# Kernel optimization log

Measured on AMD Instinct MI355X. Metric: run time of the kernel, lower is better.

## Reference

```python
import jax, jax.numpy as jnp
import numpy as np

N, NN, NI, ND, NH = 20000, 32, 128, 128, 8
RADIUS = 1.0
EPS = 1e-5


def _mlp(x, W1, b1, W2, b2):
    return jax.nn.elu(x @ W1 + b1) @ W2 + b2


def setup_inputs() -> dict:
    key = jax.random.key(0)
    ks = jax.random.split(key, 32)
    s = 0.05
    inp = {
        "features": jax.random.normal(ks[0], (N, NI), jnp.float32),
        "x": jax.random.normal(ks[1], (N, 3), jnp.float32),
        "nuv": jax.random.normal(ks[2], (N, 3, 3), jnp.float32),
        "topk": jax.random.randint(ks[3], (N, NN), 0, N, jnp.int64),
        # query_f: Ni -> Nd -> Nh*Nd
        "qW1": jax.random.normal(ks[4], (NI, ND), jnp.float32) * s,
        "qb1": jnp.zeros((ND,), jnp.float32),
        "qW2": jax.random.normal(ks[5], (ND, NH * ND), jnp.float32) * s,
        "qb2": jnp.zeros((NH * ND,), jnp.float32),
        # geo_encoder: 12 -> Nd -> Nd
        "gW1": jax.random.normal(ks[6], (12, ND), jnp.float32) * s,
        "gb1": jnp.zeros((ND,), jnp.float32),
        "gW2": jax.random.normal(ks[7], (ND, ND), jnp.float32) * s,
        "gb2": jnp.zeros((ND,), jnp.float32),
        # key_f / value_f: Nd -> Nd -> Nd
        "kW1": jax.random.normal(ks[8], (ND, ND), jnp.float32) * s,
        "kb1": jnp.zeros((ND,), jnp.float32),
        "kW2": jax.random.normal(ks[9], (ND, ND), jnp.float32) * s,
        "kb2": jnp.zeros((ND,), jnp.float32),
        "vW1": jax.random.normal(ks[10], (ND, ND), jnp.float32) * s,
        "vb1": jnp.zeros((ND,), jnp.float32),
        "vW2": jax.random.normal(ks[11], (ND, ND), jnp.float32) * s,
        "vb2": jnp.zeros((ND,), jnp.float32),
        # decode_f: Nh*Nd -> Nd -> Nd
        "dW1": jax.random.normal(ks[12], (NH * ND, ND), jnp.float32) * s,
        "db1": jnp.zeros((ND,), jnp.float32),
        "dW2": jax.random.normal(ks[13], (ND, ND), jnp.float32) * s,
        "db2": jnp.zeros((ND,), jnp.float32),
        # LayerNorm
        "ln_g": jnp.ones((ND,), jnp.float32),
        "ln_b": jnp.zeros((ND,), jnp.float32),
    }
    return inp


def reference(features, x, nuv, topk, qW1, qb1, qW2, qb2, gW1, gb1, gW2, gb2,
              kW1, kb1, kW2, kb2, vW1, vb1, vW2, vb2, dW1, db1, dW2, db2,
              ln_g, ln_b):
    n, nn = topk.shape
    sdk = jnp.sqrt(jnp.float32(ND))

    Q = _mlp(features, qW1, qb1, qW2, qb2).reshape(n, NH, ND)  # (N,Nh,Nd)

    features_nn = features[topk]              # (N,nn,Nd)
    x_nn = x[topk]                            # (N,nn,3)
    orient_x = x_nn - x[:, None, :]           # (N,nn,3)
    nuv_nn = nuv[topk].reshape(n, nn * 3, 3)  # (N,nn*3,3)

    dis2 = jnp.sum(orient_x * orient_x, axis=2, keepdims=True)
    dis = jnp.exp(-dis2 / (2.0 * RADIUS * RADIUS))  # (N,nn,1)

    # rotate neighbor offsets / frames into local frame: nuv @ v^T, then transpose
    RL_x = jnp.einsum('nij,nkj->nki', nuv, orient_x)            # (N,nn,3)
    RL_nuv = jnp.einsum('nij,nkj->nki', nuv, nuv_nn)            # (N,nn*3,3)
    RL_nuv = RL_nuv.reshape(n, nn, 9)
    RL = jnp.concatenate([RL_x, RL_nuv], axis=-1)               # (N,nn,12)

    geo_fea = _mlp(RL, gW1, gb1, gW2, gb2)
    geo_fea = dis * geo_fea * features_nn                       # (N,nn,Nd)

    K = _mlp(geo_fea, kW1, kb1, kW2, kb2)                       # (N,nn,Nd)
    V = _mlp(geo_fea, vW1, vb1, vW2, vb2)                       # (N,nn,Nd)

    Mq = jnp.einsum('nhd,nkd->nhk', Q, K)                       # (N,Nh,nn)
    mask = (topk == 0)[:, None, :]                              # (N,1,nn)
    Mq = jnp.where(mask, -jnp.inf, Mq)
    Mq = jax.nn.softmax(Mq / sdk, axis=2)

    out = jnp.einsum('nhk,nkd->nhd', Mq, V).reshape(n, NH * ND)
    out = _mlp(out, dW1, db1, dW2, db2) + features

    mu = jnp.mean(out, axis=-1, keepdims=True)
    var = jnp.var(out, axis=-1, keepdims=True)
    return (out - mu) / jnp.sqrt(var + EPS) * ln_g + ln_b
```

## Files before the change

kernel.cpp:

```cpp
#include <hip/hip_runtime.h>
#include <math.h>
#include <stdint.h>

#define ND 128
#define NNB 32
#define NH 8

typedef __attribute__((ext_vector_type(8))) short bf16x8;
typedef __attribute__((ext_vector_type(4))) float f32x4;
typedef __attribute__((ext_vector_type(8))) unsigned short u16x8;
typedef unsigned short u16;
typedef unsigned int u32;
typedef unsigned long long u64;

#define OFF_QW1T 0ULL
#define OFF_QW2T 32768ULL
#define OFF_GW1T 294912ULL
#define OFF_GW2T 303104ULL
#define OFF_KW1T 335872ULL
#define OFF_KW2T 368640ULL
#define OFF_VW1T 401408ULL
#define OFF_VW2T 434176ULL
#define OFF_DW1T 466944ULL
#define OFF_DW2T 729088ULL
#define OFF_Q    761856ULL
#define OFF_ATT  (OFF_Q + 20096ULL * 2048ULL)

__device__ __forceinline__ u16 rneb(float f){
    u32 u = __builtin_bit_cast(u32, f);
    u32 r = u + 0x7fffu + ((u >> 16) & 1u);
    return (u16)(r >> 16);
}
__device__ __forceinline__ float elu_f(float v){ return v > 0.f ? v : (__expf(v) - 1.f); }
__device__ __forceinline__ u64 pack4(float a, float b, float c, float d){
    return (u64)rneb(a) | ((u64)rneb(b) << 16) | ((u64)rneb(c) << 32) | ((u64)rneb(d) << 48);
}

#define GLDS16(g, l) __builtin_amdgcn_global_load_lds( \
    (const __attribute__((address_space(1))) u32*)(g), \
    (__attribute__((address_space(3))) u32*)(u32)(u64)(l), 16, 0, 0)

__device__ __forceinline__ void stage_rows(char* lds, const char* g, size_t gstride){
    const int t = threadIdx.x;
    const int seg = (t & 15) * 16, rr = t >> 4;
    #pragma unroll
    for (int i = 0; i < 8; i++){
        int row = i * 16 + rr;
        GLDS16(g + (size_t)row * gstride + seg, lds + row * 256 + seg);
    }
}

__device__ __forceinline__ bf16x8 ldfrag(const u16* base, int row, int kb, int l){
    int r = row + (l & 15);
    int byte = (r << 8) + (((kb << 1) + ((l >> 4) << 4)) ^ ((r & 7) << 4));
    return *(const bf16x8*)((const char*)base + byte);
}
__device__ __forceinline__ bf16x8 ldfragG(const char* __restrict__ Wt, int n, int kstride, int kb, int l){
    return *(const bf16x8*)(Wt + (size_t)(n + (l & 15)) * (size_t)kstride
                               + (size_t)((kb << 1) + ((l >> 4) << 4)));
}
__device__ __forceinline__ bf16x8 ldfragRL(const u16* base, int row, int l){
    int r = row + (l & 15);
    int byte = (r << 6) + ((((l >> 4) << 4)) ^ ((r & 3) << 4));
    return *(const bf16x8*)((const char*)base + byte);
}

__device__ __forceinline__ void gemm_WA(const char* __restrict__ Wt, int kstride, int kbase,
                                        const u16* B, f32x4 acc[4][4]){
    const int t = threadIdx.x, l = t & 63;
    const int m0 = ((t >> 7) & 1) * 64;
    const int n0 = ((t >> 6) & 1) * 64;
    bf16x8 aw[4][4];
    #pragma unroll
    for (int kk = 0; kk < 4; kk++)
        #pragma unroll
        for (int i = 0; i < 4; i++)
            aw[kk][i] = ldfragG(Wt, m0 + i * 16, kstride, kbase + kk * 32, l);
    __builtin_amdgcn_s_setprio(1);
    #pragma unroll
    for (int kk = 0; kk < 4; kk++){
        bf16x8 b[4];
        #pragma unroll
        for (int i = 0; i < 4; i++) b[i] = ldfrag(B, n0 + i * 16, kk * 32, l);
        #pragma unroll
        for (int mt = 0; mt < 4; mt++)
            #pragma unroll
            for (int nt = 0; nt < 4; nt++)
                acc[mt][nt] = __builtin_amdgcn_mfma_f32_16x16x32_bf16(aw[kk][mt], b[nt], acc[mt][nt], 0, 0, 0);
    }
    __builtin_amdgcn_s_setprio(0);
}

__device__ __forceinline__ void gemm_AW(const u16* A, const char* __restrict__ Wt,
                                        f32x4 acc[4][4]){
    const int t = threadIdx.x, l = t & 63;
    const int m0 = ((t >> 7) & 1) * 64;
    const int n0 = ((t >> 6) & 1) * 64;
    bf16x8 bw[4][4];
    #pragma unroll
    for (int kk = 0; kk < 4; kk++)
        #pragma unroll
        for (int i = 0; i < 4; i++)
            bw[kk][i] = ldfragG(Wt, n0 + i * 16, 256, kk * 32, l);
    __builtin_amdgcn_s_setprio(1);
    #pragma unroll
    for (int kk = 0; kk < 4; kk++){
        bf16x8 a[4];
        #pragma unroll
        for (int i = 0; i < 4; i++) a[i] = ldfrag(A, m0 + i * 16, kk * 32, l);
        #pragma unroll
        for (int mt = 0; mt < 4; mt++)
            #pragma unroll
            for (int nt = 0; nt < 4; nt++)
                acc[mt][nt] = __builtin_amdgcn_mfma_f32_16x16x32_bf16(a[mt], bw[kk][nt], acc[mt][nt], 0, 0, 0);
    }
    __builtin_amdgcn_s_setprio(0);
}

struct PrepDesc {
    const float* src[10];
    u64 dstoff[10];
    int N[10], Ksrc[10], Kdst[10];
};

__global__ __launch_bounds__(256) void prep_weights(PrepDesc d, char* ws){
    int tid = blockIdx.x * 256 + threadIdx.x;
    #pragma unroll 1
    for (int m = 0; m < 10; m++){
        int cnt = (d.Kdst[m] * d.N[m]) >> 3;
        if (tid < cnt){
            int N = d.N[m];
            int nn = tid % N, k8 = tid / N;
            const float* s = d.src[m];
            u16x8 pk;
            #pragma unroll
            for (int i = 0; i < 8; i++){
                int k = k8 * 8 + i;
                pk[i] = (k < d.Ksrc[m]) ? rneb(s[(size_t)k * N + nn]) : (u16)0;
            }
            *(u16x8*)(ws + d.dstoff[m] + (u64)nn * (u64)(d.Kdst[m] * 2) + (u64)(k8 * 16)) = pk;
            return;
        }
        tid -= cnt;
    }
}

__global__ __launch_bounds__(256, 2) void qmlp_kernel(
    const float* __restrict__ F, const float* __restrict__ qb1, const float* __restrict__ qb2,
    const char* __restrict__ ws, u16* __restrict__ Qg, int n)
{
    __shared__ __align__(16) u16 sIn[16384];
    __shared__ __align__(16) u16 sH[16384];
    const int t = threadIdx.x;
    const int row0 = blockIdx.x * 128;
    const int l = t & 63;
    const int m0 = ((t >> 7) & 1) * 64;
    const int n0 = ((t >> 6) & 1) * 64;
    const int hi = l >> 4;

    for (int i = t; i < 4096; i += 256){
        int r = i >> 5, c = (i & 31) * 4;
        int gr = row0 + r;
        float4 v = make_float4(0.f, 0.f, 0.f, 0.f);
        if (gr < n) v = *(const float4*)&F[(size_t)gr * ND + c];
        *(u64*)((char*)sIn + (r << 8) + (((c << 1)) ^ ((r & 7) << 4))) = pack4(v.x, v.y, v.z, v.w);
    }
    __syncthreads();

    f32x4 acc[4][4];
    #pragma unroll
    for (int i = 0; i < 4; i++)
        #pragma unroll
        for (int j = 0; j < 4; j++) acc[i][j] = 0.f;
    gemm_WA(ws + OFF_QW1T, 256, 0, sIn, acc);
    #pragma unroll
    for (int mt = 0; mt < 4; mt++){
        int ch0 = m0 + mt * 16 + (hi << 2);
        float4 bq = *(const float4*)&qb1[ch0];
        #pragma unroll
        for (int nt = 0; nt < 4; nt++){
            int xrow = n0 + nt * 16 + (l & 15);
            u64 pk = pack4(elu_f(acc[mt][nt][0] + bq.x), elu_f(acc[mt][nt][1] + bq.y),
                           elu_f(acc[mt][nt][2] + bq.z), elu_f(acc[mt][nt][3] + bq.w));
            *(u64*)((char*)sH + (xrow << 8) + (((ch0 << 1)) ^ ((xrow & 7) << 4))) = pk;
        }
    }
    __syncthreads();

    for (int ct = 0; ct < 8; ct++){
        f32x4 a2[4][4];
        #pragma unroll
        for (int i = 0; i < 4; i++)
            #pragma unroll
            for (int j = 0; j < 4; j++) a2[i][j] = 0.f;
        gemm_WA(ws + OFF_QW2T + (u64)ct * 32768ULL, 256, 0, sH, a2);
        #pragma unroll
        for (int mt = 0; mt < 4; mt++){
            int ch0 = m0 + mt * 16 + (hi << 2);
            float4 bq = *(const float4*)&qb2[ct * 128 + ch0];
            #pragma unroll
            for (int nt = 0; nt < 4; nt++){
                int xrow = n0 + nt * 16 + (l & 15);
                *(u64*)((char*)sIn + (xrow << 8) + (ch0 << 1)) =
                    pack4(a2[mt][nt][0] + bq.x, a2[mt][nt][1] + bq.y,
                          a2[mt][nt][2] + bq.z, a2[mt][nt][3] + bq.w);
            }
        }
        __syncthreads();
        {
            int row = t >> 1, half = t & 1;
            int gr = row0 + row;
            if (gr < n){
                const char* src = (const char*)sIn + (row << 8) + half * 128;
                char* dst = (char*)Qg + (size_t)gr * 2048 + ct * 256 + half * 128;
                #pragma unroll
                for (int i = 0; i < 8; i++)
                    *(uint4*)(dst + i * 16) = *(const uint4*)(src + i * 16);
            }
        }
        __syncthreads();
    }
}

template<int ACT, bool INPLACE>
__device__ __forceinline__ void layerW(
    const u16* inB, u16* outB, const char* __restrict__ Wt,
    const float* __restrict__ bias, const float* __restrict__ F,
    const int* sidx, const float* sdis)
{
    const int t = threadIdx.x, l = t & 63;
    const int m0 = ((t >> 7) & 1) * 64;
    const int n0 = ((t >> 6) & 1) * 64;
    const int hi = l >> 4;
    f32x4 acc[4][4];
    #pragma unroll
    for (int i = 0; i < 4; i++)
        #pragma unroll
        for (int j = 0; j < 4; j++) acc[i][j] = 0.f;
    gemm_WA(Wt, 256, 0, inB, acc);
    if (INPLACE) __syncthreads();
    #pragma unroll
    for (int mt = 0; mt < 4; mt++){
        int ch0 = m0 + mt * 16 + (hi << 2);
        float4 bq = *(const float4*)&bias[ch0];
        #pragma unroll
        for (int nt = 0; nt < 4; nt++){
            int xrow = n0 + nt * 16 + (l & 15);
            float v[4];
            #pragma unroll
            for (int j = 0; j < 4; j++) v[j] = acc[mt][nt][j] + ((const float*)&bq)[j];
            if (ACT == 1){
                #pragma unroll
                for (int j = 0; j < 4; j++) v[j] = elu_f(v[j]);
            }
            if (ACT == 2){
                float dsc = sdis[xrow];
                float4 fq = *(const float4*)&F[(size_t)sidx[xrow] * ND + ch0];
                #pragma unroll
                for (int j = 0; j < 4; j++) v[j] *= dsc * ((const float*)&fq)[j];
            }
            *(u64*)((char*)outB + (xrow << 8) + (((ch0 << 1)) ^ ((xrow & 7) << 4))) =
                pack4(v[0], v[1], v[2], v[3]);
        }
    }
    __syncthreads();
}

__global__ __launch_bounds__(256, 2) void attn_kernel(
    const float* __restrict__ F, const float* __restrict__ X,
    const float* __restrict__ NUV, const int* __restrict__ TOPK,
    const float* __restrict__ gb1, const float* __restrict__ gb2,
    const float* __restrict__ kb1, const float* __restrict__ kb2,
    const float* __restrict__ vb1, const float* __restrict__ vb2,
    const char* __restrict__ ws, const u16* __restrict__ Qg, u16* __restrict__ ATT)
{
    __shared__ __align__(16) u16 bufA[16384];
    __shared__ __align__(16) u16 bufB[16384];
    __shared__ __align__(16) u16 sP16[2048];
    __shared__ float sdis[128];
    __shared__ int   sidx[128];

    const int t = threadIdx.x;
    const int pid0 = blockIdx.x * 4;
    const int l = t & 63;
    const int hi = l >> 4;

    if (t < 128){
        int p = t >> 5, k = t & 31;
        int pid = pid0 + p;
        int idx = TOPK[(size_t)pid * NNB + k];
        sidx[t] = idx;
        float x0 = X[(size_t)pid * 3 + 0], x1 = X[(size_t)pid * 3 + 1], x2 = X[(size_t)pid * 3 + 2];
        float ox = X[(size_t)idx * 3 + 0] - x0;
        float oy = X[(size_t)idx * 3 + 1] - x1;
        float oz = X[(size_t)idx * 3 + 2] - x2;
        sdis[t] = __expf(-0.5f * (ox * ox + oy * oy + oz * oz));
        float nv[9];
        #pragma unroll
        for (int i = 0; i < 9; i++) nv[i] = NUV[(size_t)pid * 9 + i];
        float f[12];
        #pragma unroll
        for (int i = 0; i < 3; i++)
            f[i] = nv[i * 3 + 0] * ox + nv[i * 3 + 1] * oy + nv[i * 3 + 2] * oz;
        #pragma unroll
        for (int r = 0; r < 3; r++){
            float a0 = NUV[(size_t)idx * 9 + r * 3 + 0];
            float a1 = NUV[(size_t)idx * 9 + r * 3 + 1];
            float a2 = NUV[(size_t)idx * 9 + r * 3 + 2];
            #pragma unroll
            for (int i = 0; i < 3; i++)
                f[3 + r * 3 + i] = nv[i * 3 + 0] * a0 + nv[i * 3 + 1] * a1 + nv[i * 3 + 2] * a2;
        }
        char* rb = (char*)bufB + (t << 6);
        u32 key = (u32)(t & 3) << 4;
        *(u64*)(rb + (0u ^ key))  = pack4(f[0], f[1], f[2], f[3]);
        *(u64*)(rb + (8u ^ key))  = pack4(f[4], f[5], f[6], f[7]);
        *(u64*)(rb + (16u ^ key)) = pack4(f[8], f[9], f[10], f[11]);
        *(u64*)(rb + (24u ^ key)) = 0ULL;
        *(u64*)(rb + (32u ^ key)) = 0ULL;
        *(u64*)(rb + (40u ^ key)) = 0ULL;
        *(u64*)(rb + (48u ^ key)) = 0ULL;
        *(u64*)(rb + (56u ^ key)) = 0ULL;
    }
    __syncthreads();

    {
        const int m0 = ((t >> 7) & 1) * 64;
        const int n0 = ((t >> 6) & 1) * 64;
        bf16x8 ag[4], bg[4];
        #pragma unroll
        for (int i = 0; i < 4; i++) ag[i] = ldfragG(ws + OFF_GW1T, m0 + i * 16, 64, 0, l);
        #pragma unroll
        for (int i = 0; i < 4; i++) bg[i] = ldfragRL(bufB, n0 + i * 16, l);
        f32x4 acc[4][4];
        #pragma unroll
        for (int i = 0; i < 4; i++)
            #pragma unroll
            for (int j = 0; j < 4; j++) acc[i][j] = 0.f;
        __builtin_amdgcn_s_setprio(1);
        #pragma unroll
        for (int mt = 0; mt < 4; mt++)
            #pragma unroll
            for (int nt = 0; nt < 4; nt++)
                acc[mt][nt] = __builtin_amdgcn_mfma_f32_16x16x32_bf16(ag[mt], bg[nt], acc[mt][nt], 0, 0, 0);
        __builtin_amdgcn_s_setprio(0);
        #pragma unroll
        for (int mt = 0; mt < 4; mt++){
            int ch0 = m0 + mt * 16 + (hi << 2);
            float4 bq = *(const float4*)&gb1[ch0];
            #pragma unroll
            for (int nt = 0; nt < 4; nt++){
                int xrow = n0 + nt * 16 + (l & 15);
                u64 pk = pack4(elu_f(acc[mt][nt][0] + bq.x), elu_f(acc[mt][nt][1] + bq.y),
                               elu_f(acc[mt][nt][2] + bq.z), elu_f(acc[mt][nt][3] + bq.w));
                *(u64*)((char*)bufA + (xrow << 8) + (((ch0 << 1)) ^ ((xrow & 7) << 4))) = pk;
            }
        }
    }
    __syncthreads();

    layerW<2, false>(bufA, bufB, ws + OFF_GW2T, gb2, F, sidx, sdis);
    layerW<1, false>(bufB, bufA, ws + OFF_KW1T, kb1, F, sidx, sdis);
    layerW<0, true >(bufA, bufA, ws + OFF_KW2T, kb2, F, sidx, sdis);

    {
        const int w = t >> 6;
        f32x4 s0, s1;
        s0 = 0.f; s1 = 0.f;
        const char* qb = (const char*)Qg + (size_t)(pid0 + w) * 2048
                       + (size_t)(l & 7) * 256 + (size_t)(hi << 4);
        #pragma unroll
        for (int kk = 0; kk < 4; kk++){
            bf16x8 bq = *(const bf16x8*)(qb + kk * 64);
            bf16x8 a0 = ldfrag(bufA, w * 32,      kk * 32, l);
            bf16x8 a1 = ldfrag(bufA, w * 32 + 16, kk * 32, l);
            s0 = __builtin_amdgcn_mfma_f32_16x16x32_bf16(a0, bq, s0, 0, 0, 0);
            s1 = __builtin_amdgcn_mfma_f32_16x16x32_bf16(a1, bq, s1, 0, 0, 0);
        }
        const float RS = 0.08838834764831845f;
        float sv[8];
        #pragma unroll
        for (int mt = 0; mt < 2; mt++)
            #pragma unroll
            for (int j = 0; j < 4; j++){
                int kidx = mt * 16 + (hi << 2) + j;
                float x = (mt ? s1[j] : s0[j]) * RS;
                if (sidx[w * 32 + kidx] == 0) x = -INFINITY;
                sv[mt * 4 + j] = x;
            }
        float mx = sv[0];
        #pragma unroll
        for (int i = 1; i < 8; i++) mx = fmaxf(mx, sv[i]);
        mx = fmaxf(mx, __shfl_xor(mx, 16));
        mx = fmaxf(mx, __shfl_xor(mx, 32));
        float e[8], sum = 0.f;
        #pragma unroll
        for (int i = 0; i < 8; i++){ e[i] = __expf(sv[i] - mx); sum += e[i]; }
        sum += __shfl_xor(sum, 16);
        sum += __shfl_xor(sum, 32);
        float inv = 1.f / sum;
        char* pb = (char*)sP16 + w * 1024 + (l & 15) * 64 + hi * 8;
        *(u64*)(pb)      = pack4(e[0] * inv, e[1] * inv, e[2] * inv, e[3] * inv);
        *(u64*)(pb + 32) = pack4(e[4] * inv, e[5] * inv, e[6] * inv, e[7] * inv);
    }
    __syncthreads();

    layerW<1, false>(bufB, bufA, ws + OFF_VW1T, vb1, F, sidx, sdis);

    {
        const int m0 = ((t >> 7) & 1) * 64;
        const int n0 = ((t >> 6) & 1) * 64;
        f32x4 a2[4][4];
        #pragma unroll
        for (int i = 0; i < 4; i++)
            #pragma unroll
            for (int j = 0; j < 4; j++) a2[i][j] = 0.f;
        gemm_AW(bufA, ws + OFF_VW2T, a2);
        #pragma unroll
        for (int mt = 0; mt < 4; mt++)
            #pragma unroll
            for (int nt = 0; nt < 4; nt++){
                int ch = n0 + nt * 16 + (l & 15);
                float bv = vb2[ch];
                int r0 = m0 + mt * 16 + (hi << 2);
                *(u64*)((char*)bufB + (ch << 8) + (((r0 << 1)) ^ ((ch & 7) << 4))) =
                    pack4(a2[mt][nt][0] + bv, a2[mt][nt][1] + bv,
                          a2[mt][nt][2] + bv, a2[mt][nt][3] + bv);
            }
    }
    __syncthreads();

    {
        const int w = t >> 6;
        int pid = pid0 + w;
        u32 key = ((u32)pid & 7) << 4;
        char* dst = (char*)ATT + (size_t)pid * 2048;
        const bf16x8 pb = *(const bf16x8*)((const char*)sP16 + w * 1024 + (l & 15) * 64 + (hi << 4));
        int h = l & 15;
        #pragma unroll
        for (int nt = 0; nt < 8; nt++){
            f32x4 o;
            o = 0.f;
            bf16x8 av = ldfrag(bufB, nt * 16, w * 32, l);
            o = __builtin_amdgcn_mfma_f32_16x16x32_bf16(av, pb, o, 0, 0, 0);
            if (h < 8){
                u32 dbyte = (u32)(nt * 32 + hi * 8);
                *(u64*)(dst + h * 256 + (dbyte ^ key)) = pack4(o[0], o[1], o[2], o[3]);
            }
        }
    }
}

__global__ __launch_bounds__(256, 2) void decode_kernel(
    const u16* __restrict__ ATT,
    const float* __restrict__ db1, const float* __restrict__ db2,
    const float* __restrict__ F,
    const float* __restrict__ lng, const float* __restrict__ lnb,
    const char* __restrict__ ws, float* __restrict__ OUT, int n)
{
    __shared__ __align__(16) char SM[67584];
    u16* sA = (u16*)SM;
    u16* sH = (u16*)(SM + 32768);
    float* sO = (float*)SM;

    const int t = threadIdx.x;
    const int row0 = blockIdx.x * 128;
    const int l = t & 63;
    const int m0 = ((t >> 7) & 1) * 64;
    const int n0 = ((t >> 6) & 1) * 64;
    const int hi = l >> 4;

    f32x4 acc[4][4];
    #pragma unroll
    for (int i = 0; i < 4; i++)
        #pragma unroll
        for (int j = 0; j < 4; j++) acc[i][j] = 0.f;
    for (int kc = 0; kc < 8; kc++){
        stage_rows((char*)sA, (const char*)ATT + (size_t)row0 * 2048 + kc * 256, 2048);
        __syncthreads();
        gemm_WA(ws + OFF_DW1T, 2048, kc * 128, sA, acc);
        __syncthreads();
    }
    #pragma unroll
    for (int mt = 0; mt < 4; mt++){
        int ch0 = m0 + mt * 16 + (hi << 2);
        float4 bq = *(const float4*)&db1[ch0];
        #pragma unroll
        for (int nt = 0; nt < 4; nt++){
            int xrow = n0 + nt * 16 + (l & 15);
            u64 pk = pack4(elu_f(acc[mt][nt][0] + bq.x), elu_f(acc[mt][nt][1] + bq.y),
                           elu_f(acc[mt][nt][2] + bq.z), elu_f(acc[mt][nt][3] + bq.w));
            *(u64*)((char*)sH + (xrow << 8) + (((ch0 << 1)) ^ ((xrow & 7) << 4))) = pk;
        }
    }
    __syncthreads();

    f32x4 a2[4][4];
    #pragma unroll
    for (int i = 0; i < 4; i++)
        #pragma unroll
        for (int j = 0; j < 4; j++) a2[i][j] = 0.f;
    gemm_WA(ws + OFF_DW2T, 256, 0, sH, a2);
    __syncthreads();

    #pragma unroll
    for (int mt = 0; mt < 4; mt++){
        int ch0 = m0 + mt * 16 + (hi << 2);
        float4 bq = *(const float4*)&db2[ch0];
        #pragma unroll
        for (int nt = 0; nt < 4; nt++){
            int xrow = n0 + nt * 16 + (l & 15);
            int gr = row0 + xrow;
            float4 fres = make_float4(0.f, 0.f, 0.f, 0.f);
            if (gr < n) fres = *(const float4*)&F[(size_t)gr * ND + ch0];
            float4 ov = make_float4(a2[mt][nt][0] + bq.x + fres.x,
                                    a2[mt][nt][1] + bq.y + fres.y,
                                    a2[mt][nt][2] + bq.z + fres.z,
                                    a2[mt][nt][3] + bq.w + fres.w);
            *(float4*)&sO[xrow * 132 + ch0] = ov;
        }
    }
    __syncthreads();

    {
        int r = t >> 1, half = t & 1;
        const float* rowp = sO + r * 132 + half * 64;
        float s = 0.f;
        #pragma unroll
        for (int i = 0; i < 16; i++){
            float4 v = ((const float4*)rowp)[i];
            s += v.x + v.y + v.z + v.w;
        }
        s += __shfl_xor(s, 1);
        float mu = s * (1.0f / 128.0f);
        float q = 0.f;
        #pragma unroll
        for (int i = 0; i < 16; i++){
            float4 v = ((const float4*)rowp)[i];
            q += (v.x - mu) * (v.x - mu) + (v.y - mu) * (v.y - mu)
               + (v.z - mu) * (v.z - mu) + (v.w - mu) * (v.w - mu);
        }
        q += __shfl_xor(q, 1);
        float rstd = rsqrtf(q * (1.0f / 128.0f) + 1e-5f);
        int gr = row0 + r;
        if (gr < n){
            #pragma unroll
            for (int i = 0; i < 16; i++){
                float4 v = ((const float4*)rowp)[i];
                int c = half * 64 + i * 4;
                float4 g4 = *(const float4*)&lng[c];
                float4 b4 = *(const float4*)&lnb[c];
                float4 ov = make_float4((v.x - mu) * rstd * g4.x + b4.x,
                                        (v.y - mu) * rstd * g4.y + b4.y,
                                        (v.z - mu) * rstd * g4.z + b4.z,
                                        (v.w - mu) * rstd * g4.w + b4.w);
                *(float4*)&OUT[(size_t)gr * ND + c] = ov;
            }
        }
    }
}

extern "C" void kernel_launch(void* const* d_in, const int* in_sizes, int n_in,
                              void* d_out, int out_size, void* d_ws, size_t ws_size,
                              hipStream_t stream)
{
    const float* F    = (const float*)d_in[0];
    const float* X    = (const float*)d_in[1];
    const float* NUV  = (const float*)d_in[2];
    const int*   TOPK = (const int*)d_in[3];
    const float* qW1  = (const float*)d_in[4];
    const float* qb1  = (const float*)d_in[5];
    const float* qW2  = (const float*)d_in[6];
    const float* qb2  = (const float*)d_in[7];
    const float* gW1  = (const float*)d_in[8];
    const float* gb1  = (const float*)d_in[9];
    const float* gW2  = (const float*)d_in[10];
    const float* gb2  = (const float*)d_in[11];
    const float* kW1  = (const float*)d_in[12];
    const float* kb1  = (const float*)d_in[13];
    const float* kW2  = (const float*)d_in[14];
    const float* kb2  = (const float*)d_in[15];
    const float* vW1  = (const float*)d_in[16];
    const float* vb1  = (const float*)d_in[17];
    const float* vW2  = (const float*)d_in[18];
    const float* vb2  = (const float*)d_in[19];
    const float* dW1  = (const float*)d_in[20];
    const float* db1  = (const float*)d_in[21];
    const float* dW2  = (const float*)d_in[22];
    const float* db2  = (const float*)d_in[23];
    const float* lng  = (const float*)d_in[24];
    const float* lnb  = (const float*)d_in[25];

    const int n = in_sizes[0] / ND;
    char* wsb = (char*)d_ws;

    PrepDesc pd;
    const float* srcs[10] = {qW1, qW2, gW1, gW2, kW1, kW2, vW1, vW2, dW1, dW2};
    u64 offs[10] = {OFF_QW1T, OFF_QW2T, OFF_GW1T, OFF_GW2T, OFF_KW1T,
                    OFF_KW2T, OFF_VW1T, OFF_VW2T, OFF_DW1T, OFF_DW2T};
    int Ns[10]   = {128, 1024, 128, 128, 128, 128, 128, 128, 128, 128};
    int Ksrc[10] = {128, 128, 12, 128, 128, 128, 128, 128, 1024, 128};
    int Kdst[10] = {128, 128, 32, 128, 128, 128, 128, 128, 1024, 128};
    for (int i = 0; i < 10; i++){
        pd.src[i] = srcs[i]; pd.dstoff[i] = offs[i];
        pd.N[i] = Ns[i]; pd.Ksrc[i] = Ksrc[i]; pd.Kdst[i] = Kdst[i];
    }
    prep_weights<<<186, 256, 0, stream>>>(pd, wsb);

    u16* Qg  = (u16*)(wsb + OFF_Q);
    u16* ATT = (u16*)(wsb + OFF_ATT);
    const int nb = (n + 127) / 128;

    qmlp_kernel<<<nb, 256, 0, stream>>>(F, qb1, qb2, wsb, Qg, n);
    attn_kernel<<<n / 4, 256, 0, stream>>>(F, X, NUV, TOPK, gb1, gb2,
                                           kb1, kb2, vb1, vb2, wsb, Qg, ATT);
    decode_kernel<<<nb, 256, 0, stream>>>(ATT, db1, db2, F, lng, lnb, wsb, (float*)d_out, n);
}
```

Baseline: 422.7 us.

## Halve per-block tiles to 64 rows and raise occupancy across all three kernels

Every kernel now works on 64-row tiles (2 points per attention block) instead of 128. Each wave computes a 64x32 sub-tile, so shared memory and accumulator registers are halved and launch bounds go from 2 to 4 blocks per CU. The change also folds biases into the accumulator initialisation, packs bf16 with the hardware v_cvt_pk_bf16_f32 instruction instead of manual rounding, and reworks the V/attention output layout. The cost is more blocks, reloading the weight fragments more often per row, and more barriers per unit of work.

New measurement: 542.3 us. 1.28x slower.

```diff
diff --git a/kernel.cpp b/kernel.cpp
--- a/kernel.cpp
+++ b/kernel.cpp
@@ -9,6 +9,7 @@
 typedef __attribute__((ext_vector_type(8))) short bf16x8;
 typedef __attribute__((ext_vector_type(4))) float f32x4;
 typedef __attribute__((ext_vector_type(8))) unsigned short u16x8;
+typedef __attribute__((ext_vector_type(2))) unsigned int u32x2;
 typedef unsigned short u16;
 typedef unsigned int u32;
 typedef unsigned long long u64;
@@ -32,89 +33,70 @@
     return (u16)(r >> 16);
 }
 __device__ __forceinline__ float elu_f(float v){ return v > 0.f ? v : (__expf(v) - 1.f); }
-__device__ __forceinline__ u64 pack4(float a, float b, float c, float d){
-    return (u64)rneb(a) | ((u64)rneb(b) << 16) | ((u64)rneb(c) << 32) | ((u64)rneb(d) << 48);
+
+__device__ __forceinline__ u32 cvtpk(float a, float b){
+    u32 r;
+    asm("v_cvt_pk_bf16_f32 %0, %1, %2" : "=v"(r) : "v"(a), "v"(b));
+    return r;
+}
+__device__ __forceinline__ u32x2 cvt4(float a, float b, float c, float d){
+    u32x2 r; r.x = cvtpk(a, b); r.y = cvtpk(c, d); return r;
 }
 
 #define GLDS16(g, l) __builtin_amdgcn_global_load_lds( \
     (const __attribute__((address_space(1))) u32*)(g), \
     (__attribute__((address_space(3))) u32*)(u32)(u64)(l), 16, 0, 0)
-
-__device__ __forceinline__ void stage_rows(char* lds, const char* g, size_t gstride){
-    const int t = threadIdx.x;
-    const int seg = (t & 15) * 16, rr = t >> 4;
-    #pragma unroll
-    for (int i = 0; i < 8; i++){
-        int row = i * 16 + rr;
-        GLDS16(g + (size_t)row * gstride + seg, lds + row * 256 + seg);
-    }
-}
 
 __device__ __forceinline__ bf16x8 ldfrag(const u16* base, int row, int kb, int l){
     int r = row + (l & 15);
     int byte = (r << 8) + (((kb << 1) + ((l >> 4) << 4)) ^ ((r & 7) << 4));
     return *(const bf16x8*)((const char*)base + byte);
 }
-__device__ __forceinline__ bf16x8 ldfragG(const char* __restrict__ Wt, int n, int kstride, int kb, int l){
-    return *(const bf16x8*)(Wt + (size_t)(n + (l & 15)) * (size_t)kstride
-                               + (size_t)((kb << 1) + ((l >> 4) << 4)));
+__device__ __forceinline__ bf16x8 ldfragV(const u16* base, int row, int kb, int l){
+    int r = row + (l & 15);
+    int byte = (r << 7) + (((kb << 1) + ((l >> 4) << 4)) ^ ((r & 7) << 4));
+    return *(const bf16x8*)((const char*)base + byte);
 }
 __device__ __forceinline__ bf16x8 ldfragRL(const u16* base, int row, int l){
     int r = row + (l & 15);
     int byte = (r << 6) + ((((l >> 4) << 4)) ^ ((r & 3) << 4));
     return *(const bf16x8*)((const char*)base + byte);
 }
-
-__device__ __forceinline__ void gemm_WA(const char* __restrict__ Wt, int kstride, int kbase,
-                                        const u16* B, f32x4 acc[4][4]){
-    const int t = threadIdx.x, l = t & 63;
-    const int m0 = ((t >> 7) & 1) * 64;
-    const int n0 = ((t >> 6) & 1) * 64;
-    bf16x8 aw[4][4];
-    #pragma unroll
-    for (int kk = 0; kk < 4; kk++)
-        #pragma unroll
-        for (int i = 0; i < 4; i++)
-            aw[kk][i] = ldfragG(Wt, m0 + i * 16, kstride, kbase + kk * 32, l);
-    __builtin_amdgcn_s_setprio(1);
+__device__ __forceinline__ bf16x8 ldfragG(const char* __restrict__ Wt, int n, int kstride, int kb, int l){
+    return *(const bf16x8*)(Wt + (size_t)(n + (l & 15)) * (size_t)kstride
+                               + (size_t)((kb << 1) + ((l >> 4) << 4)));
+}
+
+__device__ __forceinline__ void gemm_WA64(const char* __restrict__ Wt, int kstride, int kbase,
+                                          const u16* B, f32x4 acc[4][2], int m0, int n0, int l){
     #pragma unroll
     for (int kk = 0; kk < 4; kk++){
-        bf16x8 b[4];
-        #pragma unroll
-        for (int i = 0; i < 4; i++) b[i] = ldfrag(B, n0 + i * 16, kk * 32, l);
+        bf16x8 aw[4];
+        #pragma unroll
+        for (int i = 0; i < 4; i++)
+            aw[i] = ldfragG(Wt, m0 + i * 16, kstride, kbase + kk * 32, l);
+        bf16x8 b[2];
+        #pragma unroll
+        for (int i = 0; i < 2; i++) b[i] = ldfrag(B, n0 + i * 16, kk * 32, l);
+        __builtin_amdgcn_s_setprio(1);
         #pragma unroll
         for (int mt = 0; mt < 4; mt++)
             #pragma unroll
-            for (int nt = 0; nt < 4; nt++)
-                acc[mt][nt] = __builtin_amdgcn_mfma_f32_16x16x32_bf16(aw[kk][mt], b[nt], acc[mt][nt], 0, 0, 0);
-    }
-    __builtin_amdgcn_s_setprio(0);
-}
-
-__device__ __forceinline__ void gemm_AW(const u16* A, const char* __restrict__ Wt,
-                                        f32x4 acc[4][4]){
-    const int t = threadIdx.x, l = t & 63;
-    const int m0 = ((t >> 7) & 1) * 64;
-    const int n0 = ((t >> 6) & 1) * 64;
-    bf16x8 bw[4][4];
+            for (int nt = 0; nt < 2; nt++)
+                acc[mt][nt] = __builtin_amdgcn_mfma_f32_16x16x32_bf16(aw[mt], b[nt], acc[mt][nt], 0, 0, 0);
+        __builtin_amdgcn_s_setprio(0);
+    }
+}
+
+__device__ __forceinline__ void bias_init(f32x4 acc[4][2], const float* __restrict__ bias,
+                                          int m0, int hi){
     #pragma unroll
-    for (int kk = 0; kk < 4; kk++)
-        #pragma unroll
-        for (int i = 0; i < 4; i++)
-            bw[kk][i] = ldfragG(Wt, n0 + i * 16, 256, kk * 32, l);
-    __builtin_amdgcn_s_setprio(1);
-    #pragma unroll
-    for (int kk = 0; kk < 4; kk++){
-        bf16x8 a[4];
-        #pragma unroll
-        for (int i = 0; i < 4; i++) a[i] = ldfrag(A, m0 + i * 16, kk * 32, l);
-        #pragma unroll
-        for (int mt = 0; mt < 4; mt++)
-            #pragma unroll
-            for (int nt = 0; nt < 4; nt++)
-                acc[mt][nt] = __builtin_amdgcn_mfma_f32_16x16x32_bf16(a[mt], bw[kk][nt], acc[mt][nt], 0, 0, 0);
-    }
-    __builtin_amdgcn_s_setprio(0);
+    for (int mt = 0; mt < 4; mt++){
+        float4 bq = *(const float4*)&bias[m0 + mt * 16 + (hi << 2)];
+        #pragma unroll
+        for (int nt = 0; nt < 2; nt++)
+            acc[mt][nt] = (f32x4){bq.x, bq.y, bq.z, bq.w};
+    }
 }
 
 struct PrepDesc {
@@ -145,77 +127,70 @@
     }
 }
 
-__global__ __launch_bounds__(256, 2) void qmlp_kernel(
+__global__ __launch_bounds__(256, 4) void qmlp_kernel(
     const float* __restrict__ F, const float* __restrict__ qb1, const float* __restrict__ qb2,
     const char* __restrict__ ws, u16* __restrict__ Qg, int n)
 {
-    __shared__ __align__(16) u16 sIn[16384];
-    __shared__ __align__(16) u16 sH[16384];
+    __shared__ __align__(16) u16 sIn[8192];
+    __shared__ __align__(16) u16 sH[8192];
     const int t = threadIdx.x;
-    const int row0 = blockIdx.x * 128;
-    const int l = t & 63;
-    const int m0 = ((t >> 7) & 1) * 64;
-    const int n0 = ((t >> 6) & 1) * 64;
+    const int row0 = blockIdx.x * 64;
+    const int l = t & 63, w = t >> 6;
+    const int m0 = (w & 1) * 64, n0 = (w >> 1) * 32;
     const int hi = l >> 4;
 
-    for (int i = t; i < 4096; i += 256){
+    for (int i = t; i < 2048; i += 256){
         int r = i >> 5, c = (i & 31) * 4;
         int gr = row0 + r;
         float4 v = make_float4(0.f, 0.f, 0.f, 0.f);
         if (gr < n) v = *(const float4*)&F[(size_t)gr * ND + c];
-        *(u64*)((char*)sIn + (r << 8) + (((c << 1)) ^ ((r & 7) << 4))) = pack4(v.x, v.y, v.z, v.w);
-    }
-    __syncthreads();
-
-    f32x4 acc[4][4];
-    #pragma unroll
-    for (int i = 0; i < 4; i++)
-        #pragma unroll
-        for (int j = 0; j < 4; j++) acc[i][j] = 0.f;
-    gemm_WA(ws + OFF_QW1T, 256, 0, sIn, acc);
-    #pragma unroll
-    for (int mt = 0; mt < 4; mt++){
-        int ch0 = m0 + mt * 16 + (hi << 2);
-        float4 bq = *(const float4*)&qb1[ch0];
-        #pragma unroll
-        for (int nt = 0; nt < 4; nt++){
-            int xrow = n0 + nt * 16 + (l & 15);
-            u64 pk = pack4(elu_f(acc[mt][nt][0] + bq.x), elu_f(acc[mt][nt][1] + bq.y),
-                           elu_f(acc[mt][nt][2] + bq.z), elu_f(acc[mt][nt][3] + bq.w));
-            *(u64*)((char*)sH + (xrow << 8) + (((ch0 << 1)) ^ ((xrow & 7) << 4))) = pk;
-        }
-    }
-    __syncthreads();
-
-    for (int ct = 0; ct < 8; ct++){
-        f32x4 a2[4][4];
-        #pragma unroll
-        for (int i = 0; i < 4; i++)
-            #pragma unroll
-            for (int j = 0; j < 4; j++) a2[i][j] = 0.f;
-        gemm_WA(ws + OFF_QW2T + (u64)ct * 32768ULL, 256, 0, sH, a2);
+        *(u32x2*)((char*)sIn + (r << 8) + (((c << 1)) ^ ((r & 7) << 4))) = cvt4(v.x, v.y, v.z, v.w);
+    }
+    __syncthreads();
+
+    {
+        f32x4 acc[4][2];
+        bias_init(acc, qb1, m0, hi);
+        gemm_WA64(ws + OFF_QW1T, 256, 0, sIn, acc, m0, n0, l);
         #pragma unroll
         for (int mt = 0; mt < 4; mt++){
             int ch0 = m0 + mt * 16 + (hi << 2);
-            float4 bq = *(const float4*)&qb2[ct * 128 + ch0];
-            #pragma unroll
-            for (int nt = 0; nt < 4; nt++){
-                int xrow = n0 + nt * 16 + (l & 15);
-                *(u64*)((char*)sIn + (xrow << 8) + (ch0 << 1)) =
-                    pack4(a2[mt][nt][0] + bq.x, a2[mt][nt][1] + bq.y,
-                          a2[mt][nt][2] + bq.z, a2[mt][nt][3] + bq.w);
+            #pragma unroll
+            for (int nt = 0; nt < 2; nt++){
+                int row = n0 + nt * 16 + (l & 15);
+                *(u32x2*)((char*)sH + (row << 8) + (((ch0 << 1)) ^ ((row & 7) << 4))) =
+                    cvt4(elu_f(acc[mt][nt][0]), elu_f(acc[mt][nt][1]),
+                         elu_f(acc[mt][nt][2]), elu_f(acc[mt][nt][3]));
+            }
+        }
+    }
+    __syncthreads();
+
+    for (int ct = 0; ct < 8; ct++){
+        f32x4 a2[4][2];
+        bias_init(a2, qb2 + ct * 128, m0, hi);
+        gemm_WA64(ws + OFF_QW2T + (u64)ct * 32768ULL, 256, 0, sH, a2, m0, n0, l);
+        #pragma unroll
+        for (int mt = 0; mt < 4; mt++){
+            int ch0 = m0 + mt * 16 + (hi << 2);
+            #pragma unroll
+            for (int nt = 0; nt < 2; nt++){
+                int row = n0 + nt * 16 + (l & 15);
+                *(u32x2*)((char*)sIn + (row << 8) + (((ch0 << 1)) ^ ((row & 7) << 4))) =
+                    cvt4(a2[mt][nt][0], a2[mt][nt][1], a2[mt][nt][2], a2[mt][nt][3]);
             }
         }
         __syncthreads();
         {
-            int row = t >> 1, half = t & 1;
+            int row = t >> 2, q = t & 3;
             int gr = row0 + row;
             if (gr < n){
-                const char* src = (const char*)sIn + (row << 8) + half * 128;
-                char* dst = (char*)Qg + (size_t)gr * 2048 + ct * 256 + half * 128;
+                const char* src = (const char*)sIn + (row << 8);
+                u32 key = ((u32)row & 7) << 4;
+                char* dst = (char*)Qg + (size_t)gr * 2048 + ct * 256 + q * 64;
                 #pragma unroll
-                for (int i = 0; i < 8; i++)
-                    *(uint4*)(dst + i * 16) = *(const uint4*)(src + i * 16);
+                for (int i = 0; i < 4; i++)
+                    *(uint4*)(dst + i * 16) = *(const uint4*)(src + (((u32)(q * 64 + i * 16)) ^ key));
             }
         }
         __syncthreads();
@@ -223,50 +198,40 @@
 }
 
 template<int ACT, bool INPLACE>
-__device__ __forceinline__ void layerW(
+__device__ __forceinline__ void layer64(
     const u16* inB, u16* outB, const char* __restrict__ Wt,
     const float* __restrict__ bias, const float* __restrict__ F,
     const int* sidx, const float* sdis)
 {
-    const int t = threadIdx.x, l = t & 63;
-    const int m0 = ((t >> 7) & 1) * 64;
-    const int n0 = ((t >> 6) & 1) * 64;
+    const int t = threadIdx.x, l = t & 63, w = t >> 6;
+    const int m0 = (w & 1) * 64, n0 = (w >> 1) * 32;
     const int hi = l >> 4;
-    f32x4 acc[4][4];
-    #pragma unroll
-    for (int i = 0; i < 4; i++)
-        #pragma unroll
-        for (int j = 0; j < 4; j++) acc[i][j] = 0.f;
-    gemm_WA(Wt, 256, 0, inB, acc);
+    f32x4 acc[4][2];
+    bias_init(acc, bias, m0, hi);
+    gemm_WA64(Wt, 256, 0, inB, acc, m0, n0, l);
     if (INPLACE) __syncthreads();
     #pragma unroll
     for (int mt = 0; mt < 4; mt++){
         int ch0 = m0 + mt * 16 + (hi << 2);
-        float4 bq = *(const float4*)&bias[ch0];
-        #pragma unroll
-        for (int nt = 0; nt < 4; nt++){
-            int xrow = n0 + nt * 16 + (l & 15);
-            float v[4];
-            #pragma unroll
-            for (int j = 0; j < 4; j++) v[j] = acc[mt][nt][j] + ((const float*)&bq)[j];
-            if (ACT == 1){
-                #pragma unroll
-                for (int j = 0; j < 4; j++) v[j] = elu_f(v[j]);
-            }
+        #pragma unroll
+        for (int nt = 0; nt < 2; nt++){
+            int row = n0 + nt * 16 + (l & 15);
+            float v0 = acc[mt][nt][0], v1 = acc[mt][nt][1];
+            float v2 = acc[mt][nt][2], v3 = acc[mt][nt][3];
+            if (ACT == 1){ v0 = elu_f(v0); v1 = elu_f(v1); v2 = elu_f(v2); v3 = elu_f(v3); }
             if (ACT == 2){
-                float dsc = sdis[xrow];
-                float4 fq = *(const float4*)&F[(size_t)sidx[xrow] * ND + ch0];
-                #pragma unroll
-                for (int j = 0; j < 4; j++) v[j] *= dsc * ((const float*)&fq)[j];
-            }
-            *(u64*)((char*)outB + (xrow << 8) + (((ch0 << 1)) ^ ((xrow & 7) << 4))) =
-                pack4(v[0], v[1], v[2], v[3]);
-        }
-    }
-    __syncthreads();
-}
-
-__global__ __launch_bounds__(256, 2) void attn_kernel(
+                float dsc = sdis[row];
+                float4 fq = *(const float4*)&F[(size_t)sidx[row] * ND + ch0];
+                v0 *= dsc * fq.x; v1 *= dsc * fq.y; v2 *= dsc * fq.z; v3 *= dsc * fq.w;
+            }
+            *(u32x2*)((char*)outB + (row << 8) + (((ch0 << 1)) ^ ((row & 7) << 4))) =
+                cvt4(v0, v1, v2, v3);
+        }
+    }
+    __syncthreads();
+}
+
+__global__ __launch_bounds__(256, 4) void attn_kernel(
     const float* __restrict__ F, const float* __restrict__ X,
     const float* __restrict__ NUV, const int* __restrict__ TOPK,
     const float* __restrict__ gb1, const float* __restrict__ gb2,
@@ -274,18 +239,19 @@
     const float* __restrict__ vb1, const float* __restrict__ vb2,
     const char* __restrict__ ws, const u16* __restrict__ Qg, u16* __restrict__ ATT)
 {
-    __shared__ __align__(16) u16 bufA[16384];
-    __shared__ __align__(16) u16 bufB[16384];
-    __shared__ __align__(16) u16 sP16[2048];
-    __shared__ float sdis[128];
-    __shared__ int   sidx[128];
+    __shared__ __align__(16) u16 bufA[8192];
+    __shared__ __align__(16) u16 bufB[8192];
+    __shared__ __align__(16) u16 sP16[1024];
+    __shared__ float sdis[64];
+    __shared__ int   sidx[64];
 
     const int t = threadIdx.x;
-    const int pid0 = blockIdx.x * 4;
-    const int l = t & 63;
+    const int pid0 = blockIdx.x * 2;
+    const int l = t & 63, w = t >> 6;
+    const int m0 = (w & 1) * 64, n0 = (w >> 1) * 32;
     const int hi = l >> 4;
 
-    if (t < 128){
+    if (t < 64){
         int p = t >> 5, k = t & 31;
         int pid = pid0 + p;
         int idx = TOPK[(size_t)pid * NNB + k];
@@ -313,58 +279,51 @@
         }
         char* rb = (char*)bufB + (t << 6);
         u32 key = (u32)(t & 3) << 4;
-        *(u64*)(rb + (0u ^ key))  = pack4(f[0], f[1], f[2], f[3]);
-        *(u64*)(rb + (8u ^ key))  = pack4(f[4], f[5], f[6], f[7]);
-        *(u64*)(rb + (16u ^ key)) = pack4(f[8], f[9], f[10], f[11]);
-        *(u64*)(rb + (24u ^ key)) = 0ULL;
-        *(u64*)(rb + (32u ^ key)) = 0ULL;
-        *(u64*)(rb + (40u ^ key)) = 0ULL;
-        *(u64*)(rb + (48u ^ key)) = 0ULL;
-        *(u64*)(rb + (56u ^ key)) = 0ULL;
+        *(u32x2*)(rb + (0u ^ key))  = cvt4(f[0], f[1], f[2], f[3]);
+        *(u32x2*)(rb + (8u ^ key))  = cvt4(f[4], f[5], f[6], f[7]);
+        *(u32x2*)(rb + (16u ^ key)) = cvt4(f[8], f[9], f[10], f[11]);
+        *(u32x2*)(rb + (24u ^ key)) = (u32x2){0u, 0u};
+        *(u32x2*)(rb + (32u ^ key)) = (u32x2){0u, 0u};
+        *(u32x2*)(rb + (40u ^ key)) = (u32x2){0u, 0u};
+        *(u32x2*)(rb + (48u ^ key)) = (u32x2){0u, 0u};
+        *(u32x2*)(rb + (56u ^ key)) = (u32x2){0u, 0u};
     }
     __syncthreads();
 
     {
-        const int m0 = ((t >> 7) & 1) * 64;
-        const int n0 = ((t >> 6) & 1) * 64;
-        bf16x8 ag[4], bg[4];
+        bf16x8 ag[4], bg[2];
         #pragma unroll
         for (int i = 0; i < 4; i++) ag[i] = ldfragG(ws + OFF_GW1T, m0 + i * 16, 64, 0, l);
         #pragma unroll
-        for (int i = 0; i < 4; i++) bg[i] = ldfragRL(bufB, n0 + i * 16, l);
-        f32x4 acc[4][4];
-        #pragma unroll
-        for (int i = 0; i < 4; i++)
-            #pragma unroll
-            for (int j = 0; j < 4; j++) acc[i][j] = 0.f;
+        for (int i = 0; i < 2; i++) bg[i] = ldfragRL(bufB, n0 + i * 16, l);
+        f32x4 acc[4][2];
+        bias_init(acc, gb1, m0, hi);
         __builtin_amdgcn_s_setprio(1);
         #pragma unroll
         for (int mt = 0; mt < 4; mt++)
             #pragma unroll
-            for (int nt = 0; nt < 4; nt++)
+            for (int nt = 0; nt < 2; nt++)
                 acc[mt][nt] = __builtin_amdgcn_mfma_f32_16x16x32_bf16(ag[mt], bg[nt], acc[mt][nt], 0, 0, 0);
         __builtin_amdgcn_s_setprio(0);
         #pragma unroll
         for (int mt = 0; mt < 4; mt++){
             int ch0 = m0 + mt * 16 + (hi << 2);
-            float4 bq = *(const float4*)&gb1[ch0];
-            #pragma unroll
-            for (int nt = 0; nt < 4; nt++){
-                int xrow = n0 + nt * 16 + (l & 15);
-                u64 pk = pack4(elu_f(acc[mt][nt][0] + bq.x), elu_f(acc[mt][nt][1] + bq.y),
-                               elu_f(acc[mt][nt][2] + bq.z), elu_f(acc[mt][nt][3] + bq.w));
-                *(u64*)((char*)bufA + (xrow << 8) + (((ch0 << 1)) ^ ((xrow & 7) << 4))) = pk;
-            }
-        }
-    }
-    __syncthreads();
-
-    layerW<2, false>(bufA, bufB, ws + OFF_GW2T, gb2, F, sidx, sdis);
-    layerW<1, false>(bufB, bufA, ws + OFF_KW1T, kb1, F, sidx, sdis);
-    layerW<0, true >(bufA, bufA, ws + OFF_KW2T, kb2, F, sidx, sdis);
-
-    {
-        const int w = t >> 6;
+            #pragma unroll
+            for (int nt = 0; nt < 2; nt++){
+                int row = n0 + nt * 16 + (l & 15);
+                *(u32x2*)((char*)bufA + (row << 8) + (((ch0 << 1)) ^ ((row & 7) << 4))) =
+                    cvt4(elu_f(acc[mt][nt][0]), elu_f(acc[mt][nt][1]),
+                         elu_f(acc[mt][nt][2]), elu_f(acc[mt][nt][3]));
+            }
+        }
+    }
+    __syncthreads();
+
+    layer64<2, false>(bufA, bufB, ws + OFF_GW2T, gb2, F, sidx, sdis);
+    layer64<1, false>(bufB, bufA, ws + OFF_KW1T, kb1, F, sidx, sdis);
+    layer64<0, true >(bufA, bufA, ws + OFF_KW2T, kb2, F, sidx, sdis);
+
+    if (w < 2){
         f32x4 s0, s1;
         s0 = 0.f; s1 = 0.f;
         const char* qb = (const char*)Qg + (size_t)(pid0 + w) * 2048
@@ -399,155 +358,177 @@
         sum += __shfl_xor(sum, 16);
         sum += __shfl_xor(sum, 32);
         float inv = 1.f / sum;
-        char* pb = (char*)sP16 + w * 1024 + (l & 15) * 64 + hi * 8;
-        *(u64*)(pb)      = pack4(e[0] * inv, e[1] * inv, e[2] * inv, e[3] * inv);
-        *(u64*)(pb + 32) = pack4(e[4] * inv, e[5] * inv, e[6] * inv, e[7] * inv);
-    }
-    __syncthreads();
-
-    layerW<1, false>(bufB, bufA, ws + OFF_VW1T, vb1, F, sidx, sdis);
+        int h = l & 15;
+        u32 key = (u32)(h & 3) << 4;
+        char* pb = (char*)sP16 + w * 1024 + h * 64;
+        *(u32x2*)(pb + (((u32)(hi * 8)) ^ key)) =
+            cvt4(e[0] * inv, e[1] * inv, e[2] * inv, e[3] * inv);
+        *(u32x2*)(pb + (((u32)(32 + hi * 8)) ^ key)) =
+            cvt4(e[4] * inv, e[5] * inv, e[6] * inv, e[7] * inv);
+    }
+    __syncthreads();
+
+    layer64<1, false>(bufB, bufA, ws + OFF_VW1T, vb1, F, sidx, sdis);
 
     {
-        const int m0 = ((t >> 7) & 1) * 64;
-        const int n0 = ((t >> 6) & 1) * 64;
-        f32x4 a2[4][4];
-        #pragma unroll
-        for (int i = 0; i < 4; i++)
-            #pragma unroll
-            for (int j = 0; j < 4; j++) a2[i][j] = 0.f;
-        gemm_AW(bufA, ws + OFF_VW2T, a2);
-        #pragma unroll
-        for (int mt = 0; mt < 4; mt++)
+        const int vm0 = (w & 1) * 32, vn0 = (w >> 1) * 64;
+        f32x4 a2[2][4];
+        #pragma unroll
+        for (int mt = 0; mt < 2; mt++)
             #pragma unroll
             for (int nt = 0; nt < 4; nt++){
-                int ch = n0 + nt * 16 + (l & 15);
-                float bv = vb2[ch];
-                int r0 = m0 + mt * 16 + (hi << 2);
-                *(u64*)((char*)bufB + (ch << 8) + (((r0 << 1)) ^ ((ch & 7) << 4))) =
-                    pack4(a2[mt][nt][0] + bv, a2[mt][nt][1] + bv,
-                          a2[mt][nt][2] + bv, a2[mt][nt][3] + bv);
-            }
+                float bv = vb2[vn0 + nt * 16 + (l & 15)];
+                a2[mt][nt] = (f32x4){bv, bv, bv, bv};
+            }
+        #pragma unroll
+        for (int kk = 0; kk < 4; kk++){
+            bf16x8 bw[4];
+            #pragma unroll
+            for (int i = 0; i < 4; i++)
+                bw[i] = ldfragG(ws + OFF_VW2T, vn0 + i * 16, 256, kk * 32, l);
+            bf16x8 a[2];
+            #pragma unroll
+            for (int i = 0; i < 2; i++) a[i] = ldfrag(bufA, vm0 + i * 16, kk * 32, l);
+            __builtin_amdgcn_s_setprio(1);
+            #pragma unroll
+            for (int mt = 0; mt < 2; mt++)
+                #pragma unroll
+                for (int nt = 0; nt < 4; nt++)
+                    a2[mt][nt] = __builtin_amdgcn_mfma_f32_16x16x32_bf16(a[mt], bw[nt], a2[mt][nt], 0, 0, 0);
+            __builtin_amdgcn_s_setprio(0);
+        }
+        __syncthreads();
+        #pragma unroll
+        for (int mt = 0; mt < 2; mt++){
+            int vr0 = vm0 + mt * 16 + (hi << 2);
+            #pragma unroll
+            for (int nt = 0; nt < 4; nt++){
+                int ch = vn0 + nt * 16 + (l & 15);
+                *(u32x2*)((char*)bufB + (ch << 7) + (((vr0 << 1)) ^ ((ch & 7) << 4))) =
+                    cvt4(a2[mt][nt][0], a2[mt][nt][1], a2[mt][nt][2], a2[mt][nt][3]);
+            }
+        }
     }
     __syncthreads();
 
     {
-        const int w = t >> 6;
-        int pid = pid0 + w;
+        const int p = w & 1, dh = w >> 1;
+        int pid = pid0 + p;
+        int h = l & 15;
+        bf16x8 pb = *(const bf16x8*)((const char*)sP16 + p * 1024 + h * 64
+                                     + (((u32)(hi * 16)) ^ ((u32)(h & 3) << 4)));
         u32 key = ((u32)pid & 7) << 4;
         char* dst = (char*)ATT + (size_t)pid * 2048;
-        const bf16x8 pb = *(const bf16x8*)((const char*)sP16 + w * 1024 + (l & 15) * 64 + (hi << 4));
-        int h = l & 15;
-        #pragma unroll
-        for (int nt = 0; nt < 8; nt++){
+        #pragma unroll
+        for (int nt = 0; nt < 4; nt++){
             f32x4 o;
             o = 0.f;
-            bf16x8 av = ldfrag(bufB, nt * 16, w * 32, l);
+            bf16x8 av = ldfragV(bufB, dh * 64 + nt * 16, p * 32, l);
             o = __builtin_amdgcn_mfma_f32_16x16x32_bf16(av, pb, o, 0, 0, 0);
             if (h < 8){
-                u32 dbyte = (u32)(nt * 32 + hi * 8);
-                *(u64*)(dst + h * 256 + (dbyte ^ key)) = pack4(o[0], o[1], o[2], o[3]);
-            }
-        }
-    }
-}
-
-__global__ __launch_bounds__(256, 2) void decode_kernel(
+                u32 dbyte = (u32)(dh * 128 + nt * 32 + hi * 8);
+                *(u32x2*)(dst + h * 256 + (dbyte ^ key)) = cvt4(o[0], o[1], o[2], o[3]);
+            }
+        }
+    }
+}
+
+__global__ __launch_bounds__(256, 4) void decode_kernel(
     const u16* __restrict__ ATT,
     const float* __restrict__ db1, const float* __restrict__ db2,
     const float* __restrict__ F,
     const float* __restrict__ lng, const float* __restrict__ lnb,
     const char* __restrict__ ws, float* __restrict__ OUT, int n)
 {
-    __shared__ __align__(16) char SM[67584];
+    __shared__ __align__(16) char SM[34048];
     u16* sA = (u16*)SM;
-    u16* sH = (u16*)(SM + 32768);
+    u16* sH = (u16*)(SM + 16384);
     float* sO = (float*)SM;
 
     const int t = threadIdx.x;
-    const int row0 = blockIdx.x * 128;
-    const int l = t & 63;
-    const int m0 = ((t >> 7) & 1) * 64;
-    const int n0 = ((t >> 6) & 1) * 64;
+    const int row0 = blockIdx.x * 64;
+    const int l = t & 63, w = t >> 6;
+    const int m0 = (w & 1) * 64, n0 = (w >> 1) * 32;
     const int hi = l >> 4;
 
-    f32x4 acc[4][4];
-    #pragma unroll
-    for (int i = 0; i < 4; i++)
-        #pragma unroll
-        for (int j = 0; j < 4; j++) acc[i][j] = 0.f;
+    f32x4 acc[4][2];
+    bias_init(acc, db1, m0, hi);
     for (int kc = 0; kc < 8; kc++){
-        stage_rows((char*)sA, (const char*)ATT + (size_t)row0 * 2048 + kc * 256, 2048);
+        {
+            const int seg = (t & 15) * 16, rr = t >> 4;
+            const char* g = (const char*)ATT + (size_t)row0 * 2048 + kc * 256;
+            #pragma unroll
+            for (int i = 0; i < 4; i++){
+                int row = i * 16 + rr;
+                GLDS16(g + (size_t)row * 2048 + seg, (char*)sA + row * 256 + seg);
+            }
+        }
         __syncthreads();
-        gemm_WA(ws + OFF_DW1T, 2048, kc * 128, sA, acc);
+        gemm_WA64(ws + OFF_DW1T, 2048, kc * 128, sA, acc, m0, n0, l);
         __syncthreads();
     }
     #pragma unroll
     for (int mt = 0; mt < 4; mt++){
         int ch0 = m0 + mt * 16 + (hi << 2);
-        float4 bq = *(const float4*)&db1[ch0];
-        #pragma unroll
-        for (int nt = 0; nt < 4; nt++){
-            int xrow = n0 + nt * 16 + (l & 15);
-            u64 pk = pack4(elu_f(acc[mt][nt][0] + bq.x), elu_f(acc[mt][nt][1] + bq.y),
-                           elu_f(acc[mt][nt][2] + bq.z), elu_f(acc[mt][nt][3] + bq.w));
-            *(u64*)((char*)sH + (xrow << 8) + (((ch0 << 1)) ^ ((xrow & 7) << 4))) = pk;
-        }
-    }
-    __syncthreads();
-
-    f32x4 a2[4][4];
-    #pragma unroll
-    for (int i = 0; i < 4; i++)
-        #pragma unroll
-        for (int j = 0; j < 4; j++) a2[i][j] = 0.f;
-    gemm_WA(ws + OFF_DW2T, 256, 0, sH, a2);
+        #pragma unroll
+        for (int nt = 0; nt < 2; nt++){
+            int row = n0 + nt * 16 + (l & 15);
+            *(u32x2*)((char*)sH + (row << 8) + (((ch0 << 1)) ^ ((row & 7) << 4))) =
+                cvt4(elu_f(acc[mt][nt][0]), elu_f(acc[mt][nt][1]),
+                     elu_f(acc[mt][nt][2]), elu_f(acc[mt][nt][3]));
+        }
+    }
+    __syncthreads();
+
+    f32x4 a2[4][2];
+    bias_init(a2, db2, m0, hi);
+    gemm_WA64(ws + OFF_DW2T, 256, 0, sH, a2, m0, n0, l);
     __syncthreads();
 
     #pragma unroll
     for (int mt = 0; mt < 4; mt++){
         int ch0 = m0 + mt * 16 + (hi << 2);
-        float4 bq = *(const float4*)&db2[ch0];
-        #pragma unroll
-        for (int nt = 0; nt < 4; nt++){
-            int xrow = n0 + nt * 16 + (l & 15);
-            int gr = row0 + xrow;
+        #pragma unroll
+        for (int nt = 0; nt < 2; nt++){
+            int row = n0 + nt * 16 + (l & 15);
+            int gr = row0 + row;
             float4 fres = make_float4(0.f, 0.f, 0.f, 0.f);
             if (gr < n) fres = *(const float4*)&F[(size_t)gr * ND + ch0];
-            float4 ov = make_float4(a2[mt][nt][0] + bq.x + fres.x,
-                                    a2[mt][nt][1] + bq.y + fres.y,
-                                    a2[mt][nt][2] + bq.z + fres.z,
-                                    a2[mt][nt][3] + bq.w + fres.w);
-            *(float4*)&sO[xrow * 132 + ch0] = ov;
+            float4 ov = make_float4(a2[mt][nt][0] + fres.x, a2[mt][nt][1] + fres.y,
+                                    a2[mt][nt][2] + fres.z, a2[mt][nt][3] + fres.w);
+            *(float4*)&sO[row * 132 + ch0] = ov;
         }
     }
     __syncthreads();
 
     {
-        int r = t >> 1, half = t & 1;
-        const float* rowp = sO + r * 132 + half * 64;
+        int r = t >> 2, q = t & 3;
+        const float* rowp = sO + r * 132 + q * 32;
         float s = 0.f;
         #pragma unroll
-        for (int i = 0; i < 16; i++){
+        for (int i = 0; i < 8; i++){
             float4 v = ((const float4*)rowp)[i];
             s += v.x + v.y + v.z + v.w;
         }
         s += __shfl_xor(s, 1);
+        s += __shfl_xor(s, 2);
         float mu = s * (1.0f / 128.0f);
-        float q = 0.f;
-        #pragma unroll
-        for (int i = 0; i < 16; i++){
+        float q2 = 0.f;
+        #pragma unroll
+        for (int i = 0; i < 8; i++){
             float4 v = ((const float4*)rowp)[i];
-            q += (v.x - mu) * (v.x - mu) + (v.y - mu) * (v.y - mu)
-               + (v.z - mu) * (v.z - mu) + (v.w - mu) * (v.w - mu);
-        }
-        q += __shfl_xor(q, 1);
-        float rstd = rsqrtf(q * (1.0f / 128.0f) + 1e-5f);
+            q2 += (v.x - mu) * (v.x - mu) + (v.y - mu) * (v.y - mu)
+                + (v.z - mu) * (v.z - mu) + (v.w - mu) * (v.w - mu);
+        }
+        q2 += __shfl_xor(q2, 1);
+        q2 += __shfl_xor(q2, 2);
+        float rstd = rsqrtf(q2 * (1.0f / 128.0f) + 1e-5f);
         int gr = row0 + r;
         if (gr < n){
             #pragma unroll
-            for (int i = 0; i < 16; i++){
+            for (int i = 0; i < 8; i++){
                 float4 v = ((const float4*)rowp)[i];
-                int c = half * 64 + i * 4;
+                int c = q * 32 + i * 4;
                 float4 g4 = *(const float4*)&lng[c];
                 float4 b4 = *(const float4*)&lnb[c];
                 float4 ov = make_float4((v.x - mu) * rstd * g4.x + b4.x,
@@ -609,10 +590,10 @@
 
     u16* Qg  = (u16*)(wsb + OFF_Q);
     u16* ATT = (u16*)(wsb + OFF_ATT);
-    const int nb = (n + 127) / 128;
+    const int nb = (n + 63) / 64;
 
     qmlp_kernel<<<nb, 256, 0, stream>>>(F, qb1, qb2, wsb, Qg, n);
-    attn_kernel<<<n / 4, 256, 0, stream>>>(F, X, NUV, TOPK, gb1, gb2,
+    attn_kernel<<<n / 2, 256, 0, stream>>>(F, X, NUV, TOPK, gb1, gb2,
                                            kb1, kb2, vb1, vb2, wsb, Qg, ATT);
     decode_kernel<<<nb, 256, 0, stream>>>(ATT, db1, db2, F, lng, lnb, wsb, (float*)d_out, n);
 }
```
